# Optimization experiments

Hardware: AMD Instinct MI355X
Metric: run time of the kernel (lower is better)

Reference implementation:

```python
import jax, jax.numpy as jnp
import numpy as np

B, N = 16, 512            # graphs, atoms per graph
F_DIM, H, D = 128, 64, 16  # feature_dim, hidden_dim, far_source_dim
CUT, GROWTH = 5.0, 2.0
NS, NT = 3, 2
MULT = GROWTH ** NS        # default far_max_radius_multiplier = 8
EMAX = CUT * MULT          # 40.0
TOT = NS + NT              # 5 shells total
SF = D + 3                 # 19 per-shell features
SE_IN = TOT * SF           # 95
EH_IN = 4 * D + SE_IN      # 159
N_RBF = 8
BOUNDS = [(5.0, 10.0), (10.0, 20.0), (20.0, 40.0), (40.0, 80.0), (80.0, float('inf'))]


def ln(x, g, b):
    m = x.mean(-1, keepdims=True)
    v = x.var(-1, keepdims=True)
    return (x - m) / jnp.sqrt(v + 1e-5) * g + b


def setup_inputs() -> dict:
    key = jax.random.key(0)
    ks = jax.random.split(key, 16)
    W = lambda k, i, o: jax.random.normal(k, (i, o), jnp.float32) / np.sqrt(i)
    inp = {}
    inp['x'] = jax.random.normal(ks[0], (B * N, F_DIM), jnp.float32)
    inp['pos'] = jax.random.uniform(ks[1], (B * N, 3), jnp.float32) * 80.0
    inp['batch'] = jnp.repeat(jnp.arange(B, dtype=jnp.int32), N)
    inp['num_graphs'] = B
    inp['in_ln_g'] = jnp.ones(F_DIM); inp['in_ln_b'] = jnp.zeros(F_DIM)
    inp['src_w1'] = W(ks[2], F_DIM, H); inp['src_b1'] = jnp.zeros(H)
    inp['src_w2'] = W(ks[3], H, D);     inp['src_b2'] = jnp.zeros(D)
    inp['src_ln_g'] = jnp.ones(D); inp['src_ln_b'] = jnp.zeros(D)
    inp['se_ln_g'] = jnp.ones(SE_IN); inp['se_ln_b'] = jnp.zeros(SE_IN)
    inp['se_w1'] = W(ks[4], SE_IN, H); inp['se_b1'] = jnp.zeros(H)
    inp['se_w2'] = W(ks[5], H, D);     inp['se_b2'] = jnp.zeros(D)
    inp['eh_ln_g'] = jnp.ones(EH_IN); inp['eh_ln_b'] = jnp.zeros(EH_IN)
    inp['eh_w1'] = W(ks[6], EH_IN, H); inp['eh_b1'] = jnp.zeros(H)
    inp['eh_w2'] = W(ks[7], H, 1);     inp['eh_b2'] = jnp.zeros(1)
    inp['k_screen'] = jnp.float32(-8.0)
    inp['kg_w1'] = W(ks[8], N_RBF + 2, 32); inp['kg_b1'] = jnp.zeros(32)
    inp['kg_w2'] = jnp.zeros((32, 1)); inp['kg_b2'] = jnp.zeros(1)  # zero-init per source
    inp['far_gate'] = jnp.float32(0.2)
    inp['energy_scale'] = jnp.float32(0.0)
    return inp


def reference(x, pos, batch, num_graphs, in_ln_g, in_ln_b, src_w1, src_b1, src_w2, src_b2,
              src_ln_g, src_ln_b, se_ln_g, se_ln_b, se_w1, se_b1, se_w2, se_b2,
              eh_ln_g, eh_ln_b, eh_w1, eh_b1, eh_w2, eh_b2,
              k_screen, kg_w1, kg_b1, kg_w2, kg_b2, far_gate, energy_scale):
    M = x.shape[0]
    n = M // num_graphs
    # per-atom source features
    h = ln(x, in_ln_g, in_ln_b)
    src = jax.nn.silu(h @ src_w1 + src_b1) @ src_w2 + src_b2
    src = ln(src, src_ln_g, src_ln_b)
    # graph-wise neutralization (subtract per-graph mean)
    gsum = jax.ops.segment_sum(src, batch, num_segments=num_graphs)
    cnt = jax.ops.segment_sum(jnp.ones((M, 1), x.dtype), batch, num_segments=num_graphs)
    src = src - (gsum / jnp.maximum(cnt, 1.0))[batch]
    # pairwise distances per graph
    p = pos.reshape(num_graphs, n, 3)
    s = src.reshape(num_graphs, n, D)
    diff = p[:, :, None, :] - p[:, None, :, :]
    d = jnp.sqrt((diff * diff).sum(-1) + 1e-12)  # [B,n,n]
    not_self = ~jnp.eye(n, dtype=bool)[None]
    # physical kernel with learned RBF gate
    screening = jax.nn.softplus(k_screen)
    base = jnp.exp(-screening * d) / jnp.maximum(d, 1e-6)
    centers = jnp.linspace(CUT, EMAX, N_RBF)
    spacing = (EMAX - CUT) / (N_RBF - 1)
    gamma = 1.0 / (spacing * spacing)
    dc = d[..., None]
    rbf = jnp.exp(-gamma * (dc - centers) ** 2)
    gin = jnp.concatenate([dc / CUT, dc / EMAX, rbf], -1)
    gate = 1.0 + jnp.tanh(jax.nn.silu(gin @ kg_w1 + kg_b1) @ kg_w2 + kg_b2)[..., 0]
    ker = base * gate
    # shell statistics: kernel-weighted mean source, count, mean_r, rms_r per shell
    feats = []
    for lo, up in BOUNDS:
        m = (d >= lo) & not_self
        if np.isfinite(up):
            m = m & (d < up)
        mf = m.astype(x.dtype)
        c = mf.sum(-1)
        denom = jnp.maximum(c, 1.0)
        mean = jnp.einsum('bij,bjc->bic', ker * mf, s) / denom[..., None]
        mr = (mf * d).sum(-1) / denom
        rr = jnp.sqrt((mf * d * d).sum(-1) / denom + 1e-12)
        feats.append(jnp.concatenate([mean, c[..., None], mr[..., None], rr[..., None]], -1))
    shell = jnp.concatenate(feats, -1).reshape(M, SE_IN)  # [M, 95]
    emb = jax.nn.silu(ln(shell, se_ln_g, se_ln_b) @ se_w1 + se_b1) @ se_w2 + se_b2
    ein = jnp.concatenate([src, emb, src * emb, src - emb, shell], -1)  # [M, 159]
    pa = (jax.nn.silu(ln(ein, eh_ln_g, eh_ln_b) @ eh_w1 + eh_b1) @ eh_w2 + eh_b2)[..., 0]
    pa = pa * jnp.tanh(far_gate) * jnp.exp(energy_scale)
    return jax.ops.segment_sum(pa, batch, num_segments=num_graphs)  # per-graph energies [B]
```

## Files before the change

kernel.cpp:

```cpp
#include <hip/hip_runtime.h>
#include <math.h>

#define B_G   16
#define N_A   512
#define M_AT  8192
#define FD    128
#define HD    64
#define DD    16
#define SEIN  95
#define EHIN  159
#define NLUT  512
#define DMAXF 140.0f
#define NFB   512

__device__ __forceinline__ float silu_f(float z) { return z / (1.f + __expf(-z)); }

__global__ __launch_bounds__(256) void k_front(
    const float* __restrict__ x,
    const float* __restrict__ g, const float* __restrict__ bb,
    const float* __restrict__ w1, const float* __restrict__ b1,
    const float* __restrict__ w2, const float* __restrict__ b2,
    const float* __restrict__ lng, const float* __restrict__ lnb,
    const float* __restrict__ k_screen,
    const float* __restrict__ kg_w1, const float* __restrict__ kg_b1,
    const float* __restrict__ kg_w2, const float* __restrict__ kg_b2,
    float* __restrict__ srcout, float* __restrict__ partials,
    float2* __restrict__ lut, float* __restrict__ out) {
  int t = threadIdx.x;

  if (blockIdx.x >= NFB) {
    int lb = blockIdx.x - NFB;
    __shared__ float w1l[320], b1l[32], w2l[32];
    if (lb == 0 && t < B_G) out[t] = 0.f;
    for (int idx = t; idx < 320; idx += 256) w1l[idx] = kg_w1[idx];
    if (t < 32) { b1l[t] = kg_b1[t]; w2l[t] = kg_w2[t]; }
    __syncthreads();
    int i = lb * 256 + t;
    float step = DMAXF / (float)(NLUT - 1);
    float ksv = k_screen[0];
    float screening = fmaxf(ksv, 0.f) + log1pf(expf(-fabsf(ksv)));
    float b2v = kg_b2[0];
    float vals[2];
#pragma unroll
    for (int e = 0; e < 2; ++e) {
      int ii = min(i + e, NLUT - 1);
      float d = (float)ii * step;
      float base = expf(-screening * d) / fmaxf(d, 1e-6f);
      float gin[10];
      gin[0] = d * (1.f / 5.0f);
      gin[1] = d * (1.f / 40.0f);
#pragma unroll
      for (int kk = 0; kk < 8; ++kk) {
        float u = d - (5.0f + 5.0f * (float)kk);
        gin[2 + kk] = expf(-(1.f / 25.f) * u * u);
      }
      float accv = 0.f;
      for (int h = 0; h < 32; ++h) {
        float z = b1l[h];
#pragma unroll
        for (int kk = 0; kk < 10; ++kk) z += gin[kk] * w1l[kk * 32 + h];
        accv += silu_f(z) * w2l[h];
      }
      vals[e] = base * (1.f + tanhf(accv + b2v));
    }
    lut[i] = make_float2(vals[0], vals[1] - vals[0]);
    return;
  }

  int wave = t >> 6, lane = t & 63;
  int ag = lane >> 4, l16 = lane & 15;
  int a = wave * 4 + ag;
  int atom = blockIdx.x * 16 + a;

  __shared__ __align__(16) float xn[16 * 132];
  __shared__ __align__(16) float hb[16 * 68];
  __shared__ float psum[4][16];

  float xr[8];
  {
    const float4* xp = (const float4*)(x + (size_t)atom * FD + l16 * 8);
    float4 v0 = xp[0], v1 = xp[1];
    xr[0] = v0.x; xr[1] = v0.y; xr[2] = v0.z; xr[3] = v0.w;
    xr[4] = v1.x; xr[5] = v1.y; xr[6] = v1.z; xr[7] = v1.w;
  }
  float s = 0.f;
#pragma unroll
  for (int i = 0; i < 8; ++i) s += xr[i];
  s += __shfl_xor(s, 1); s += __shfl_xor(s, 2); s += __shfl_xor(s, 4); s += __shfl_xor(s, 8);
  float m = s * (1.f / 128.f);
  float v2 = 0.f;
#pragma unroll
  for (int i = 0; i < 8; ++i) { float d = xr[i] - m; v2 += d * d; }
  v2 += __shfl_xor(v2, 1); v2 += __shfl_xor(v2, 2); v2 += __shfl_xor(v2, 4); v2 += __shfl_xor(v2, 8);
  float inv = rsqrtf(v2 * (1.f / 128.f) + 1e-5f);
  {
    int kb = l16 * 8;
    float4 gv0 = ((const float4*)g)[l16 * 2], gv1 = ((const float4*)g)[l16 * 2 + 1];
    float4 bv0 = ((const float4*)bb)[l16 * 2], bv1 = ((const float4*)bb)[l16 * 2 + 1];
    float4 o0, o1;
    o0.x = (xr[0] - m) * inv * gv0.x + bv0.x;
    o0.y = (xr[1] - m) * inv * gv0.y + bv0.y;
    o0.z = (xr[2] - m) * inv * gv0.z + bv0.z;
    o0.w = (xr[3] - m) * inv * gv0.w + bv0.w;
    o1.x = (xr[4] - m) * inv * gv1.x + bv1.x;
    o1.y = (xr[5] - m) * inv * gv1.y + bv1.y;
    o1.z = (xr[6] - m) * inv * gv1.z + bv1.z;
    o1.w = (xr[7] - m) * inv * gv1.w + bv1.w;
    *(float4*)&xn[a * 132 + kb] = o0;
    *(float4*)&xn[a * 132 + kb + 4] = o1;
  }
  __syncthreads();

  float acc[4] = {0.f, 0.f, 0.f, 0.f};
  {
    const float* xnb = &xn[a * 132];
#pragma unroll 4
    for (int k = 0; k < FD; k += 4) {
      float4 xa = *(const float4*)(xnb + k);
      float4 wa = ((const float4*)(w1 + (size_t)(k + 0) * HD))[l16];
      float4 wbv = ((const float4*)(w1 + (size_t)(k + 1) * HD))[l16];
      float4 wc = ((const float4*)(w1 + (size_t)(k + 2) * HD))[l16];
      float4 wd = ((const float4*)(w1 + (size_t)(k + 3) * HD))[l16];
      acc[0] += wa.x * xa.x; acc[0] += wbv.x * xa.y; acc[0] += wc.x * xa.z; acc[0] += wd.x * xa.w;
      acc[1] += wa.y * xa.x; acc[1] += wbv.y * xa.y; acc[1] += wc.y * xa.z; acc[1] += wd.y * xa.w;
      acc[2] += wa.z * xa.x; acc[2] += wbv.z * xa.y; acc[2] += wc.z * xa.z; acc[2] += wd.z * xa.w;
      acc[3] += wa.w * xa.x; acc[3] += wbv.w * xa.y; acc[3] += wc.w * xa.z; acc[3] += wd.w * xa.w;
    }
    float4 bv = ((const float4*)b1)[l16];
    float4 ho;
    ho.x = silu_f(acc[0] + bv.x); ho.y = silu_f(acc[1] + bv.y);
    ho.z = silu_f(acc[2] + bv.z); ho.w = silu_f(acc[3] + bv.w);
    *(float4*)&hb[a * 68 + l16 * 4] = ho;
  }
  __syncthreads();

  {
    float acc2 = 0.f;
    const float* hbb = &hb[a * 68];
#pragma unroll
    for (int h = 0; h < HD; h += 4) {
      float4 hv = *(const float4*)(hbb + h);
      acc2 += w2[(h + 0) * DD + l16] * hv.x;
      acc2 += w2[(h + 1) * DD + l16] * hv.y;
      acc2 += w2[(h + 2) * DD + l16] * hv.z;
      acc2 += w2[(h + 3) * DD + l16] * hv.w;
    }
    float val = acc2 + b2[l16];
    float sm = val;
    sm += __shfl_xor(sm, 1); sm += __shfl_xor(sm, 2); sm += __shfl_xor(sm, 4); sm += __shfl_xor(sm, 8);
    float mm = sm * (1.f / 16.f);
    float dv = val - mm;
    float vv = dv * dv;
    vv += __shfl_xor(vv, 1); vv += __shfl_xor(vv, 2); vv += __shfl_xor(vv, 4); vv += __shfl_xor(vv, 8);
    float iv = rsqrtf(vv * (1.f / 16.f) + 1e-5f);
    float ov = dv * iv * lng[l16] + lnb[l16];
    srcout[(size_t)atom * DD + l16] = ov;
    float lsum = ov;
    lsum += __shfl_xor(lsum, 16); lsum += __shfl_xor(lsum, 32);
    if (lane < 16) psum[wave][l16] = lsum;
  }
  __syncthreads();
  if (t < 16)
    partials[(size_t)blockIdx.x * 16 + t] =
        psum[0][t] + psum[1][t] + psum[2][t] + psum[3][t];
}

__global__ __launch_bounds__(256) void k_pairs(
    const float* __restrict__ pos, const float* __restrict__ src,
    const float2* __restrict__ lut, const float* __restrict__ partials,
    float* __restrict__ shell) {
  int gph = blockIdx.x >> 7;
  int blk = blockIdx.x & 127;
  int t = threadIdx.x, wave = t >> 6, lane = t & 63;
  int i_local = blk * 4 + wave;

  __shared__ __align__(16) float ss[N_A * DD];
  __shared__ __align__(16) float2 luts[NLUT];
  __shared__ __align__(16) unsigned wb[4][N_A];
  __shared__ float smean[16];

  const float* posg = pos + (size_t)gph * N_A * 3;

  for (int idx = t; idx < N_A * DD / 4; idx += 256)
    ((float4*)ss)[idx] = ((const float4*)(src + (size_t)gph * N_A * DD))[idx];
  if (t < NLUT / 2) ((float4*)luts)[t] = ((const float4*)lut)[t];
  if (t < 64) {
    int c = t & 15, grp = t >> 4;
    float sm = 0.f;
#pragma unroll
    for (int k = 0; k < 8; ++k)
      sm += partials[(size_t)(gph * 32 + grp * 8 + k) * 16 + c];
    sm += __shfl_xor(sm, 16); sm += __shfl_xor(sm, 32);
    if (t < 16) smean[c] = sm * (1.f / 512.f);
  }

  float px = posg[i_local * 3], py = posg[i_local * 3 + 1], pz = posg[i_local * 3 + 2];
  __syncthreads();

  float cnt[5] = {0,0,0,0,0}, sd[5] = {0,0,0,0,0}, sdd[5] = {0,0,0,0,0}, sw[5] = {0,0,0,0,0};
  const float lscale = (float)(NLUT - 1) / DMAXF;

#pragma unroll
  for (int it = 0; it < 8; ++it) {
    int jv = lane + it * 64;
    float qx = posg[jv * 3], qy = posg[jv * 3 + 1], qz = posg[jv * 3 + 2];
    float dx = px - qx, dy = py - qy, dz = pz - qz;
    float d2 = dx * dx + dy * dy + dz * dz + 1e-12f;
    float d = sqrtf(d2);
    bool valid = (jv != i_local) && (d >= 5.0f);
    int tq = (d >= 10.f) + (d >= 20.f) + (d >= 40.f) + (d >= 80.f);
    float xq = d * lscale;
    int i0 = min((int)xq, NLUT - 2);
    float f = xq - (float)i0;
    float2 L = luts[i0];
    float w = valid ? (L.x + L.y * f) : 0.f;
    wb[wave][jv] = (__float_as_uint(w) & ~7u) | (unsigned)tq;
    float dm = valid ? d : 0.f;
    float ddm = valid ? d * d : 0.f;
    float cm = valid ? 1.f : 0.f;
#pragma unroll
    for (int q = 0; q < 5; ++q) {
      bool mq = (tq == q);
      cnt[q] += mq ? cm : 0.f;
      sd[q]  += mq ? dm : 0.f;
      sdd[q] += mq ? ddm : 0.f;
      sw[q]  += mq ? w : 0.f;
    }
  }
#pragma unroll
  for (int q = 0; q < 5; ++q) {
#pragma unroll
    for (int o = 32; o > 0; o >>= 1) {
      cnt[q] += __shfl_xor(cnt[q], o);
      sd[q]  += __shfl_xor(sd[q], o);
      sdd[q] += __shfl_xor(sdd[q], o);
      sw[q]  += __shfl_xor(sw[q], o);
    }
  }
  __syncthreads();

  int cq = lane & 3, jlow = lane >> 2;
  float accq[5][4] = {};
  const float* ssb = &ss[jlow * DD + cq * 4];
  const unsigned* wbb = &wb[wave][jlow];
#pragma unroll
  for (int jj = 0; jj < 32; ++jj) {
    float4 sv = *(const float4*)(ssb + jj * 256);
    unsigned u = wbb[jj * 16];
    int tq = (int)(u & 7u);
    float w = __uint_as_float(u & ~7u);
    float w0 = (tq == 0) ? w : 0.f;
    float w1_ = (tq == 1) ? w : 0.f;
    float w2_ = (tq == 2) ? w : 0.f;
    float w3_ = (tq == 3) ? w : 0.f;
    float w4_ = (tq == 4) ? w : 0.f;
    accq[0][0] += w0 * sv.x; accq[0][1] += w0 * sv.y; accq[0][2] += w0 * sv.z; accq[0][3] += w0 * sv.w;
    accq[1][0] += w1_ * sv.x; accq[1][1] += w1_ * sv.y; accq[1][2] += w1_ * sv.z; accq[1][3] += w1_ * sv.w;
    accq[2][0] += w2_ * sv.x; accq[2][1] += w2_ * sv.y; accq[2][2] += w2_ * sv.z; accq[2][3] += w2_ * sv.w;
    accq[3][0] += w3_ * sv.x; accq[3][1] += w3_ * sv.y; accq[3][2] += w3_ * sv.z; accq[3][3] += w3_ * sv.w;
    accq[4][0] += w4_ * sv.x; accq[4][1] += w4_ * sv.y; accq[4][2] += w4_ * sv.z; accq[4][3] += w4_ * sv.w;
  }
#pragma unroll
  for (int q = 0; q < 5; ++q)
#pragma unroll
    for (int i = 0; i < 4; ++i) {
      float v = accq[q][i];
      v += __shfl_xor(v, 4); v += __shfl_xor(v, 8); v += __shfl_xor(v, 16); v += __shfl_xor(v, 32);
      accq[q][i] = v;
    }

  float* shp = shell + (size_t)(gph * N_A + i_local) * SEIN;
  if (jlow == 0) {
#pragma unroll
    for (int q = 0; q < 5; ++q) {
      float denom = fmaxf(cnt[q], 1.f);
#pragma unroll
      for (int i = 0; i < 4; ++i) {
        int c = cq * 4 + i;
        shp[q * 19 + c] = (accq[q][i] - smean[c] * sw[q]) / denom;
      }
    }
  }
  if (lane < 5) {
    int q = lane;
    float denom = fmaxf(cnt[q], 1.f);
    shp[q * 19 + 16] = cnt[q];
    shp[q * 19 + 17] = sd[q] / denom;
    shp[q * 19 + 18] = sqrtf(sdd[q] / denom + 1e-12f);
  }
}

__global__ __launch_bounds__(256) void k_tail(
    const float* __restrict__ src, const float* __restrict__ shell,
    const float* __restrict__ partials,
    const float* __restrict__ se_ln_g, const float* __restrict__ se_ln_b,
    const float* __restrict__ se_w1, const float* __restrict__ se_b1,
    const float* __restrict__ se_w2, const float* __restrict__ se_b2,
    const float* __restrict__ eh_ln_g, const float* __restrict__ eh_ln_b,
    const float* __restrict__ eh_w1, const float* __restrict__ eh_b1,
    const float* __restrict__ eh_w2, const float* __restrict__ eh_b2,
    const float* __restrict__ far_gate, const float* __restrict__ energy_scale,
    float* __restrict__ out) {
  int t = threadIdx.x, wave = t >> 6, lane = t & 63;
  int ag = lane >> 4, l16 = lane & 15;
  int a = wave * 4 + ag;
  int aB = blockIdx.x * 16;
  int gph = aB >> 9;

  __shared__ __align__(16) float ein[16 * 160];
  __shared__ __align__(16) float shn[16 * 96];
  __shared__ __align__(16) float hb[16 * 68];
  __shared__ float smean[16];
  __shared__ float redv[4];

  if (t < 64) {
    int c = t & 15, grp = t >> 4;
    float sm = 0.f;
#pragma unroll
    for (int k = 0; k < 8; ++k)
      sm += partials[(size_t)(gph * 32 + grp * 8 + k) * 16 + c];
    sm += __shfl_xor(sm, 16); sm += __shfl_xor(sm, 32);
    if (t < 16) smean[c] = sm * (1.f / 512.f);
  }

  const float* shg = shell + (size_t)aB * SEIN;
  for (int idx = t; idx < 16 * SEIN; idx += 256) {
    unsigned a_loc = ((unsigned)idx * 690u) >> 16;
    int kk = idx - (int)a_loc * SEIN;
    ein[a_loc * 160 + 64 + kk] = shg[idx];
  }
  __syncthreads();

  {
    float s1 = 0.f, sq = 0.f;
    const float* eb = &ein[a * 160 + 64];
#pragma unroll
    for (int i = 0; i < 6; ++i) {
      int k = l16 * 6 + i;
      if (k < SEIN) { float v = eb[k]; s1 += v; sq += v * v; }
    }
    s1 += __shfl_xor(s1, 1); s1 += __shfl_xor(s1, 2); s1 += __shfl_xor(s1, 4); s1 += __shfl_xor(s1, 8);
    sq += __shfl_xor(sq, 1); sq += __shfl_xor(sq, 2); sq += __shfl_xor(sq, 4); sq += __shfl_xor(sq, 8);
    float m = s1 * (1.f / (float)SEIN);
    float var = sq * (1.f / (float)SEIN) - m * m;
    float inv = rsqrtf(var + 1e-5f);
#pragma unroll
    for (int i = 0; i < 6; ++i) {
      int k = l16 * 6 + i;
      if (k < SEIN)
        shn[a * 96 + k] = (eb[k] - m) * inv * se_ln_g[k] + se_ln_b[k];
    }
  }
  __syncthreads();

  int h0 = l16 * 4;
  {
    float acc[4] = {0.f, 0.f, 0.f, 0.f};
    const float* sb = &shn[a * 96];
#pragma unroll 4
    for (int k = 0; k < 92; k += 4) {
      float4 xa = *(const float4*)(sb + k);
      float4 wa = ((const float4*)(se_w1 + (size_t)(k + 0) * HD))[l16];
      float4 wbv = ((const float4*)(se_w1 + (size_t)(k + 1) * HD))[l16];
      float4 wc = ((const float4*)(se_w1 + (size_t)(k + 2) * HD))[l16];
      float4 wd = ((const float4*)(se_w1 + (size_t)(k + 3) * HD))[l16];
      acc[0] += wa.x * xa.x; acc[0] += wbv.x * xa.y; acc[0] += wc.x * xa.z; acc[0] += wd.x * xa.w;
      acc[1] += wa.y * xa.x; acc[1] += wbv.y * xa.y; acc[1] += wc.y * xa.z; acc[1] += wd.y * xa.w;
      acc[2] += wa.z * xa.x; acc[2] += wbv.z * xa.y; acc[2] += wc.z * xa.z; acc[2] += wd.z * xa.w;
      acc[3] += wa.w * xa.x; acc[3] += wbv.w * xa.y; acc[3] += wc.w * xa.z; acc[3] += wd.w * xa.w;
    }
#pragma unroll
    for (int k = 92; k < SEIN; ++k) {
      float xa = sb[k];
      float4 wa = ((const float4*)(se_w1 + (size_t)k * HD))[l16];
      acc[0] += wa.x * xa; acc[1] += wa.y * xa; acc[2] += wa.z * xa; acc[3] += wa.w * xa;
    }
    float4 bv = ((const float4*)se_b1)[l16];
    float4 ho;
    ho.x = silu_f(acc[0] + bv.x); ho.y = silu_f(acc[1] + bv.y);
    ho.z = silu_f(acc[2] + bv.z); ho.w = silu_f(acc[3] + bv.w);
    *(float4*)&hb[a * 68 + h0] = ho;
  }
  __syncthreads();

  {
    float acc2 = 0.f;
    const float* hbb = &hb[a * 68];
#pragma unroll
    for (int h = 0; h < HD; h += 4) {
      float4 hv = *(const float4*)(hbb + h);
      acc2 += se_w2[(h + 0) * DD + l16] * hv.x;
      acc2 += se_w2[(h + 1) * DD + l16] * hv.y;
      acc2 += se_w2[(h + 2) * DD + l16] * hv.z;
      acc2 += se_w2[(h + 3) * DD + l16] * hv.w;
    }
    float ev = acc2 + se_b2[l16];
    float sv = src[(size_t)(aB + a) * DD + l16] - smean[l16];
    ein[a * 160 + l16] = sv;
    ein[a * 160 + 16 + l16] = ev;
    ein[a * 160 + 32 + l16] = sv * ev;
    ein[a * 160 + 48 + l16] = sv - ev;
  }
  __syncthreads();

  {
    float s1 = 0.f, sq = 0.f;
    float* eb = &ein[a * 160];
#pragma unroll
    for (int i = 0; i < 10; ++i) {
      int k = l16 * 10 + i;
      if (k < EHIN) { float v = eb[k]; s1 += v; sq += v * v; }
    }
    s1 += __shfl_xor(s1, 1); s1 += __shfl_xor(s1, 2); s1 += __shfl_xor(s1, 4); s1 += __shfl_xor(s1, 8);
    sq += __shfl_xor(sq, 1); sq += __shfl_xor(sq, 2); sq += __shfl_xor(sq, 4); sq += __shfl_xor(sq, 8);
    float m = s1 * (1.f / (float)EHIN);
    float var = sq * (1.f / (float)EHIN) - m * m;
    float inv = rsqrtf(var + 1e-5f);
#pragma unroll
    for (int i = 0; i < 10; ++i) {
      int k = l16 * 10 + i;
      if (k < EHIN)
        eb[k] = (eb[k] - m) * inv * eh_ln_g[k] + eh_ln_b[k];
    }
  }
  __syncthreads();

  {
    float acc[4] = {0.f, 0.f, 0.f, 0.f};
    const float* eb = &ein[a * 160];
#pragma unroll 4
    for (int k = 0; k < 156; k += 4) {
      float4 xa = *(const float4*)(eb + k);
      float4 wa = ((const float4*)(eh_w1 + (size_t)(k + 0) * HD))[l16];
      float4 wbv = ((const float4*)(eh_w1 + (size_t)(k + 1) * HD))[l16];
      float4 wc = ((const float4*)(eh_w1 + (size_t)(k + 2) * HD))[l16];
      float4 wd = ((const float4*)(eh_w1 + (size_t)(k + 3) * HD))[l16];
      acc[0] += wa.x * xa.x; acc[0] += wbv.x * xa.y; acc[0] += wc.x * xa.z; acc[0] += wd.x * xa.w;
      acc[1] += wa.y * xa.x; acc[1] += wbv.y * xa.y; acc[1] += wc.y * xa.z; acc[1] += wd.y * xa.w;
      acc[2] += wa.z * xa.x; acc[2] += wbv.z * xa.y; acc[2] += wc.z * xa.z; acc[2] += wd.z * xa.w;
      acc[3] += wa.w * xa.x; acc[3] += wbv.w * xa.y; acc[3] += wc.w * xa.z; acc[3] += wd.w * xa.w;
    }
#pragma unroll
    for (int k = 156; k < EHIN; ++k) {
      float xa = eb[k];
      float4 wa = ((const float4*)(eh_w1 + (size_t)k * HD))[l16];
      acc[0] += wa.x * xa; acc[1] += wa.y * xa; acc[2] += wa.z * xa; acc[3] += wa.w * xa;
    }
    float4 b1v = ((const float4*)eh_b1)[l16];
    float4 w2v = ((const float4*)eh_w2)[l16];
    float pa = silu_f(acc[0] + b1v.x) * w2v.x + silu_f(acc[1] + b1v.y) * w2v.y
             + silu_f(acc[2] + b1v.z) * w2v.z + silu_f(acc[3] + b1v.w) * w2v.w;
    pa += __shfl_xor(pa, 1); pa += __shfl_xor(pa, 2); pa += __shfl_xor(pa, 4); pa += __shfl_xor(pa, 8);
    pa += __shfl_xor(pa, 16); pa += __shfl_xor(pa, 32);
    if (lane == 0) redv[wave] = pa + 4.f * eh_b2[0];
  }
  __syncthreads();
  if (t == 0) {
    float tot = redv[0] + redv[1] + redv[2] + redv[3];
    atomicAdd(&out[gph], tot * tanhf(far_gate[0]) * expf(energy_scale[0]));
  }
}

extern "C" void kernel_launch(void* const* d_in, const int* in_sizes, int n_in,
                              void* d_out, int out_size, void* d_ws, size_t ws_size,
                              hipStream_t stream) {
  const float* x         = (const float*)d_in[0];
  const float* pos       = (const float*)d_in[1];
  const float* in_ln_g   = (const float*)d_in[4];
  const float* in_ln_b   = (const float*)d_in[5];
  const float* src_w1    = (const float*)d_in[6];
  const float* src_b1    = (const float*)d_in[7];
  const float* src_w2    = (const float*)d_in[8];
  const float* src_b2    = (const float*)d_in[9];
  const float* src_ln_g  = (const float*)d_in[10];
  const float* src_ln_b  = (const float*)d_in[11];
  const float* se_ln_g   = (const float*)d_in[12];
  const float* se_ln_b   = (const float*)d_in[13];
  const float* se_w1     = (const float*)d_in[14];
  const float* se_b1     = (const float*)d_in[15];
  const float* se_w2     = (const float*)d_in[16];
  const float* se_b2     = (const float*)d_in[17];
  const float* eh_ln_g   = (const float*)d_in[18];
  const float* eh_ln_b   = (const float*)d_in[19];
  const float* eh_w1     = (const float*)d_in[20];
  const float* eh_b1     = (const float*)d_in[21];
  const float* eh_w2     = (const float*)d_in[22];
  const float* eh_b2     = (const float*)d_in[23];
  const float* k_screen  = (const float*)d_in[24];
  const float* kg_w1     = (const float*)d_in[25];
  const float* kg_b1     = (const float*)d_in[26];
  const float* kg_w2     = (const float*)d_in[27];
  const float* kg_b2     = (const float*)d_in[28];
  const float* far_gate  = (const float*)d_in[29];
  const float* en_scale  = (const float*)d_in[30];
  float* out = (float*)d_out;

  float* ws_src   = (float*)d_ws;
  float* ws_shell = ws_src + (size_t)M_AT * DD;
  float* ws_part  = ws_shell + (size_t)M_AT * SEIN;
  float2* ws_lut  = (float2*)(ws_part + NFB * 16);

  k_front<<<NFB + 2, 256, 0, stream>>>(x, in_ln_g, in_ln_b, src_w1, src_b1,
                                       src_w2, src_b2, src_ln_g, src_ln_b,
                                       k_screen, kg_w1, kg_b1, kg_w2, kg_b2,
                                       ws_src, ws_part, ws_lut, out);
  k_pairs<<<B_G * (N_A / 4), 256, 0, stream>>>(pos, ws_src, ws_lut, ws_part, ws_shell);
  k_tail<<<M_AT / 16, 256, 0, stream>>>(ws_src, ws_shell, ws_part,
                                        se_ln_g, se_ln_b, se_w1, se_b1, se_w2, se_b2,
                                        eh_ln_g, eh_ln_b, eh_w1, eh_b1, eh_w2, eh_b2,
                                        far_gate, en_scale, out);
}
```

Measured before the change: 189.5 us.

## Compact per-shell neighbor indices with ballots and sparse-gather shell means

The old version computed the kernel-weighted shell means by looping over all 512 neighbors, doing masked multiply-adds into five shell accumulators for every neighbor. The new version first uses wave ballots and popcounts to compact the neighbor indices of each shell into a shared-memory list. It then gathers only the members of each shell, doing four FMAs per neighbor instead of twenty. The price is extra ballot passes and dependent indirect LDS loads, and the block-wide __syncthreads before this stage is dropped. The list layout assumes the number of nonzero-weight entries in each shell equals the float shell count.

```diff
diff --git a/kernel.cpp b/kernel.cpp
--- a/kernel.cpp
+++ b/kernel.cpp
@@ -177,6 +177,7 @@
   __shared__ __align__(16) float ss[N_A * DD];
   __shared__ __align__(16) float2 luts[NLUT];
   __shared__ __align__(16) unsigned wb[4][N_A];
+  __shared__ __align__(16) unsigned short jl[4][N_A];
   __shared__ float smean[16];
 
   const float* posg = pos + (size_t)gph * N_A * 3;
@@ -237,48 +238,66 @@
       sw[q]  += __shfl_xor(sw[q], o);
     }
   }
-  __syncthreads();
-
-  int cq = lane & 3, jlow = lane >> 2;
-  float accq[5][4] = {};
-  const float* ssb = &ss[jlow * DD + cq * 4];
-  const unsigned* wbb = &wb[wave][jlow];
-#pragma unroll
-  for (int jj = 0; jj < 32; ++jj) {
-    float4 sv = *(const float4*)(ssb + jj * 256);
-    unsigned u = wbb[jj * 16];
-    int tq = (int)(u & 7u);
-    float w = __uint_as_float(u & ~7u);
-    float w0 = (tq == 0) ? w : 0.f;
-    float w1_ = (tq == 1) ? w : 0.f;
-    float w2_ = (tq == 2) ? w : 0.f;
-    float w3_ = (tq == 3) ? w : 0.f;
-    float w4_ = (tq == 4) ? w : 0.f;
-    accq[0][0] += w0 * sv.x; accq[0][1] += w0 * sv.y; accq[0][2] += w0 * sv.z; accq[0][3] += w0 * sv.w;
-    accq[1][0] += w1_ * sv.x; accq[1][1] += w1_ * sv.y; accq[1][2] += w1_ * sv.z; accq[1][3] += w1_ * sv.w;
-    accq[2][0] += w2_ * sv.x; accq[2][1] += w2_ * sv.y; accq[2][2] += w2_ * sv.z; accq[2][3] += w2_ * sv.w;
-    accq[3][0] += w3_ * sv.x; accq[3][1] += w3_ * sv.y; accq[3][2] += w3_ * sv.z; accq[3][3] += w3_ * sv.w;
-    accq[4][0] += w4_ * sv.x; accq[4][1] += w4_ * sv.y; accq[4][2] += w4_ * sv.z; accq[4][3] += w4_ * sv.w;
-  }
-#pragma unroll
-  for (int q = 0; q < 5; ++q)
-#pragma unroll
-    for (int i = 0; i < 4; ++i) {
-      float v = accq[q][i];
-      v += __shfl_xor(v, 4); v += __shfl_xor(v, 8); v += __shfl_xor(v, 16); v += __shfl_xor(v, 32);
-      accq[q][i] = v;
-    }
-
+
+  int nI[5], stq[5];
+#pragma unroll
+  for (int q = 0; q < 5; ++q) nI[q] = (int)cnt[q];
+  stq[0] = 0;
+  stq[1] = nI[0];
+  stq[2] = stq[1] + nI[1];
+  stq[3] = stq[2] + nI[2];
+  stq[4] = stq[3] + nI[3];
+  {
+    int b0 = stq[0], b1 = stq[1], b2 = stq[2], b3 = stq[3], b4 = stq[4];
+    unsigned long long lt = (lane == 63) ? 0x7fffffffffffffffull
+                                         : ((1ull << lane) - 1ull);
+#pragma unroll
+    for (int it = 0; it < 8; ++it) {
+      int jv = lane + it * 64;
+      unsigned u = wb[wave][jv];
+      int tq = (int)(u & 7u);
+      bool val = (u >> 3) != 0u;
+      unsigned long long m0 = __ballot(val && tq == 0);
+      unsigned long long m1 = __ballot(val && tq == 1);
+      unsigned long long m2 = __ballot(val && tq == 2);
+      unsigned long long m3 = __ballot(val && tq == 3);
+      unsigned long long m4 = __ballot(val && tq == 4);
+      if (val) {
+        if (tq == 0)      jl[wave][b0 + __popcll(m0 & lt)] = (unsigned short)jv;
+        else if (tq == 1) jl[wave][b1 + __popcll(m1 & lt)] = (unsigned short)jv;
+        else if (tq == 2) jl[wave][b2 + __popcll(m2 & lt)] = (unsigned short)jv;
+        else if (tq == 3) jl[wave][b3 + __popcll(m3 & lt)] = (unsigned short)jv;
+        else              jl[wave][b4 + __popcll(m4 & lt)] = (unsigned short)jv;
+      }
+      b0 += __popcll(m0); b1 += __popcll(m1); b2 += __popcll(m2);
+      b3 += __popcll(m3); b4 += __popcll(m4);
+    }
+  }
+
+  int cq = lane & 3, jl16 = lane >> 2;
   float* shp = shell + (size_t)(gph * N_A + i_local) * SEIN;
-  if (jlow == 0) {
-#pragma unroll
-    for (int q = 0; q < 5; ++q) {
+#pragma unroll
+  for (int q = 0; q < 5; ++q) {
+    float a0 = 0.f, a1 = 0.f, a2 = 0.f, a3 = 0.f;
+    int n = nI[q], s0 = stq[q];
+    for (int idx = jl16; idx < n; idx += 16) {
+      int j = jl[wave][s0 + idx];
+      unsigned u = wb[wave][j];
+      float w = __uint_as_float(u & ~7u);
+      float4 sv = *(const float4*)&ss[j * DD + cq * 4];
+      a0 += w * sv.x; a1 += w * sv.y; a2 += w * sv.z; a3 += w * sv.w;
+    }
+    a0 += __shfl_xor(a0, 4); a0 += __shfl_xor(a0, 8); a0 += __shfl_xor(a0, 16); a0 += __shfl_xor(a0, 32);
+    a1 += __shfl_xor(a1, 4); a1 += __shfl_xor(a1, 8); a1 += __shfl_xor(a1, 16); a1 += __shfl_xor(a1, 32);
+    a2 += __shfl_xor(a2, 4); a2 += __shfl_xor(a2, 8); a2 += __shfl_xor(a2, 16); a2 += __shfl_xor(a2, 32);
+    a3 += __shfl_xor(a3, 4); a3 += __shfl_xor(a3, 8); a3 += __shfl_xor(a3, 16); a3 += __shfl_xor(a3, 32);
+    if (jl16 == 0) {
       float denom = fmaxf(cnt[q], 1.f);
-#pragma unroll
-      for (int i = 0; i < 4; ++i) {
-        int c = cq * 4 + i;
-        shp[q * 19 + c] = (accq[q][i] - smean[c] * sw[q]) / denom;
-      }
+      int c = cq * 4;
+      shp[q * 19 + c + 0] = (a0 - smean[c + 0] * sw[q]) / denom;
+      shp[q * 19 + c + 1] = (a1 - smean[c + 1] * sw[q]) / denom;
+      shp[q * 19 + c + 2] = (a2 - smean[c + 2] * sw[q]) / denom;
+      shp[q * 19 + c + 3] = (a3 - smean[c + 3] * sw[q]) / denom;
     }
   }
   if (lane < 5) {
```

Result: slower. 196.5 us (+3.7%).

## Fuse tail MLP heads into pair kernel, drop shell workspace round-trip

Applied to the files above, without the earlier changes.

The per-atom shell-embedding MLP and energy head now run inside k_pairs, one wave per atom, using shared-memory staging instead of writing the 95-float shell vector to global memory and launching k_tail. This removes one kernel launch and the global write and read of the shell buffer. Each wave now does both MLPs with one hidden unit per lane and scalar weight loads, which may use the lanes less efficiently than the previous 16-atom tiled tail. It also adds shared memory to k_pairs, which may lower occupancy.

```diff
diff --git a/kernel.cpp b/kernel.cpp
--- a/kernel.cpp
+++ b/kernel.cpp
@@ -168,7 +168,14 @@
 __global__ __launch_bounds__(256) void k_pairs(
     const float* __restrict__ pos, const float* __restrict__ src,
     const float2* __restrict__ lut, const float* __restrict__ partials,
-    float* __restrict__ shell) {
+    const float* __restrict__ se_ln_g, const float* __restrict__ se_ln_b,
+    const float* __restrict__ se_w1, const float* __restrict__ se_b1,
+    const float* __restrict__ se_w2, const float* __restrict__ se_b2,
+    const float* __restrict__ eh_ln_g, const float* __restrict__ eh_ln_b,
+    const float* __restrict__ eh_w1, const float* __restrict__ eh_b1,
+    const float* __restrict__ eh_w2, const float* __restrict__ eh_b2,
+    const float* __restrict__ far_gate, const float* __restrict__ energy_scale,
+    float* __restrict__ out) {
   int gph = blockIdx.x >> 7;
   int blk = blockIdx.x & 127;
   int t = threadIdx.x, wave = t >> 6, lane = t & 63;
@@ -177,7 +184,12 @@
   __shared__ __align__(16) float ss[N_A * DD];
   __shared__ __align__(16) float2 luts[NLUT];
   __shared__ __align__(16) unsigned wb[4][N_A];
+  __shared__ __align__(16) float shl[4][100];
+  __shared__ __align__(16) float shnf[4][100];
+  __shared__ __align__(16) float einf[4][164];
+  __shared__ __align__(16) float hbf[4][64];
   __shared__ float smean[16];
+  __shared__ float redv[4];
 
   const float* posg = pos + (size_t)gph * N_A * 3;
 
@@ -239,220 +251,125 @@
   }
   __syncthreads();
 
-  int cq = lane & 3, jlow = lane >> 2;
-  float accq[5][4] = {};
-  const float* ssb = &ss[jlow * DD + cq * 4];
-  const unsigned* wbb = &wb[wave][jlow];
-#pragma unroll
-  for (int jj = 0; jj < 32; ++jj) {
-    float4 sv = *(const float4*)(ssb + jj * 256);
-    unsigned u = wbb[jj * 16];
-    int tq = (int)(u & 7u);
-    float w = __uint_as_float(u & ~7u);
-    float w0 = (tq == 0) ? w : 0.f;
-    float w1_ = (tq == 1) ? w : 0.f;
-    float w2_ = (tq == 2) ? w : 0.f;
-    float w3_ = (tq == 3) ? w : 0.f;
-    float w4_ = (tq == 4) ? w : 0.f;
-    accq[0][0] += w0 * sv.x; accq[0][1] += w0 * sv.y; accq[0][2] += w0 * sv.z; accq[0][3] += w0 * sv.w;
-    accq[1][0] += w1_ * sv.x; accq[1][1] += w1_ * sv.y; accq[1][2] += w1_ * sv.z; accq[1][3] += w1_ * sv.w;
-    accq[2][0] += w2_ * sv.x; accq[2][1] += w2_ * sv.y; accq[2][2] += w2_ * sv.z; accq[2][3] += w2_ * sv.w;
-    accq[3][0] += w3_ * sv.x; accq[3][1] += w3_ * sv.y; accq[3][2] += w3_ * sv.z; accq[3][3] += w3_ * sv.w;
-    accq[4][0] += w4_ * sv.x; accq[4][1] += w4_ * sv.y; accq[4][2] += w4_ * sv.z; accq[4][3] += w4_ * sv.w;
-  }
-#pragma unroll
-  for (int q = 0; q < 5; ++q)
-#pragma unroll
-    for (int i = 0; i < 4; ++i) {
-      float v = accq[q][i];
-      v += __shfl_xor(v, 4); v += __shfl_xor(v, 8); v += __shfl_xor(v, 16); v += __shfl_xor(v, 32);
-      accq[q][i] = v;
-    }
-
-  float* shp = shell + (size_t)(gph * N_A + i_local) * SEIN;
-  if (jlow == 0) {
-#pragma unroll
-    for (int q = 0; q < 5; ++q) {
+  {
+    int cq = lane & 3, jlow = lane >> 2;
+    float accq[5][4] = {};
+    const float* ssb = &ss[jlow * DD + cq * 4];
+    const unsigned* wbb = &wb[wave][jlow];
+#pragma unroll
+    for (int jj = 0; jj < 32; ++jj) {
+      float4 sv = *(const float4*)(ssb + jj * 256);
+      unsigned u = wbb[jj * 16];
+      int tq = (int)(u & 7u);
+      float w = __uint_as_float(u & ~7u);
+      float w0 = (tq == 0) ? w : 0.f;
+      float w1_ = (tq == 1) ? w : 0.f;
+      float w2_ = (tq == 2) ? w : 0.f;
+      float w3_ = (tq == 3) ? w : 0.f;
+      float w4_ = (tq == 4) ? w : 0.f;
+      accq[0][0] += w0 * sv.x; accq[0][1] += w0 * sv.y; accq[0][2] += w0 * sv.z; accq[0][3] += w0 * sv.w;
+      accq[1][0] += w1_ * sv.x; accq[1][1] += w1_ * sv.y; accq[1][2] += w1_ * sv.z; accq[1][3] += w1_ * sv.w;
+      accq[2][0] += w2_ * sv.x; accq[2][1] += w2_ * sv.y; accq[2][2] += w2_ * sv.z; accq[2][3] += w2_ * sv.w;
+      accq[3][0] += w3_ * sv.x; accq[3][1] += w3_ * sv.y; accq[3][2] += w3_ * sv.z; accq[3][3] += w3_ * sv.w;
+      accq[4][0] += w4_ * sv.x; accq[4][1] += w4_ * sv.y; accq[4][2] += w4_ * sv.z; accq[4][3] += w4_ * sv.w;
+    }
+#pragma unroll
+    for (int q = 0; q < 5; ++q)
+#pragma unroll
+      for (int i = 0; i < 4; ++i) {
+        float v = accq[q][i];
+        v += __shfl_xor(v, 4); v += __shfl_xor(v, 8); v += __shfl_xor(v, 16); v += __shfl_xor(v, 32);
+        accq[q][i] = v;
+      }
+
+    if (jlow == 0) {
+#pragma unroll
+      for (int q = 0; q < 5; ++q) {
+        float denom = fmaxf(cnt[q], 1.f);
+#pragma unroll
+        for (int i = 0; i < 4; ++i) {
+          int c = cq * 4 + i;
+          shl[wave][q * 19 + c] = (accq[q][i] - smean[c] * sw[q]) / denom;
+        }
+      }
+    }
+    if (lane < 5) {
+      int q = lane;
       float denom = fmaxf(cnt[q], 1.f);
-#pragma unroll
-      for (int i = 0; i < 4; ++i) {
-        int c = cq * 4 + i;
-        shp[q * 19 + c] = (accq[q][i] - smean[c] * sw[q]) / denom;
-      }
-    }
-  }
-  if (lane < 5) {
-    int q = lane;
-    float denom = fmaxf(cnt[q], 1.f);
-    shp[q * 19 + 16] = cnt[q];
-    shp[q * 19 + 17] = sd[q] / denom;
-    shp[q * 19 + 18] = sqrtf(sdd[q] / denom + 1e-12f);
-  }
-}
-
-__global__ __launch_bounds__(256) void k_tail(
-    const float* __restrict__ src, const float* __restrict__ shell,
-    const float* __restrict__ partials,
-    const float* __restrict__ se_ln_g, const float* __restrict__ se_ln_b,
-    const float* __restrict__ se_w1, const float* __restrict__ se_b1,
-    const float* __restrict__ se_w2, const float* __restrict__ se_b2,
-    const float* __restrict__ eh_ln_g, const float* __restrict__ eh_ln_b,
-    const float* __restrict__ eh_w1, const float* __restrict__ eh_b1,
-    const float* __restrict__ eh_w2, const float* __restrict__ eh_b2,
-    const float* __restrict__ far_gate, const float* __restrict__ energy_scale,
-    float* __restrict__ out) {
-  int t = threadIdx.x, wave = t >> 6, lane = t & 63;
-  int ag = lane >> 4, l16 = lane & 15;
-  int a = wave * 4 + ag;
-  int aB = blockIdx.x * 16;
-  int gph = aB >> 9;
-
-  __shared__ __align__(16) float ein[16 * 160];
-  __shared__ __align__(16) float shn[16 * 96];
-  __shared__ __align__(16) float hb[16 * 68];
-  __shared__ float smean[16];
-  __shared__ float redv[4];
-
-  if (t < 64) {
-    int c = t & 15, grp = t >> 4;
-    float sm = 0.f;
-#pragma unroll
-    for (int k = 0; k < 8; ++k)
-      sm += partials[(size_t)(gph * 32 + grp * 8 + k) * 16 + c];
-    sm += __shfl_xor(sm, 16); sm += __shfl_xor(sm, 32);
-    if (t < 16) smean[c] = sm * (1.f / 512.f);
-  }
-
-  const float* shg = shell + (size_t)aB * SEIN;
-  for (int idx = t; idx < 16 * SEIN; idx += 256) {
-    unsigned a_loc = ((unsigned)idx * 690u) >> 16;
-    int kk = idx - (int)a_loc * SEIN;
-    ein[a_loc * 160 + 64 + kk] = shg[idx];
-  }
-  __syncthreads();
-
-  {
-    float s1 = 0.f, sq = 0.f;
-    const float* eb = &ein[a * 160 + 64];
-#pragma unroll
-    for (int i = 0; i < 6; ++i) {
-      int k = l16 * 6 + i;
-      if (k < SEIN) { float v = eb[k]; s1 += v; sq += v * v; }
-    }
-    s1 += __shfl_xor(s1, 1); s1 += __shfl_xor(s1, 2); s1 += __shfl_xor(s1, 4); s1 += __shfl_xor(s1, 8);
-    sq += __shfl_xor(sq, 1); sq += __shfl_xor(sq, 2); sq += __shfl_xor(sq, 4); sq += __shfl_xor(sq, 8);
+      shl[wave][q * 19 + 16] = cnt[q];
+      shl[wave][q * 19 + 17] = sd[q] / denom;
+      shl[wave][q * 19 + 18] = sqrtf(sdd[q] / denom + 1e-12f);
+    }
+  }
+  __syncthreads();
+
+  {
+    float v1 = shl[wave][lane];
+    float v2 = (lane < 31) ? shl[wave][lane + 64] : 0.f;
+    float s1 = v1 + v2, sq = v1 * v1 + v2 * v2;
+    s1 += __shfl_xor(s1, 1); s1 += __shfl_xor(s1, 2); s1 += __shfl_xor(s1, 4);
+    s1 += __shfl_xor(s1, 8); s1 += __shfl_xor(s1, 16); s1 += __shfl_xor(s1, 32);
+    sq += __shfl_xor(sq, 1); sq += __shfl_xor(sq, 2); sq += __shfl_xor(sq, 4);
+    sq += __shfl_xor(sq, 8); sq += __shfl_xor(sq, 16); sq += __shfl_xor(sq, 32);
     float m = s1 * (1.f / (float)SEIN);
     float var = sq * (1.f / (float)SEIN) - m * m;
     float inv = rsqrtf(var + 1e-5f);
-#pragma unroll
-    for (int i = 0; i < 6; ++i) {
-      int k = l16 * 6 + i;
-      if (k < SEIN)
-        shn[a * 96 + k] = (eb[k] - m) * inv * se_ln_g[k] + se_ln_b[k];
-    }
-  }
-  __syncthreads();
-
-  int h0 = l16 * 4;
-  {
-    float acc[4] = {0.f, 0.f, 0.f, 0.f};
-    const float* sb = &shn[a * 96];
-#pragma unroll 4
-    for (int k = 0; k < 92; k += 4) {
-      float4 xa = *(const float4*)(sb + k);
-      float4 wa = ((const float4*)(se_w1 + (size_t)(k + 0) * HD))[l16];
-      float4 wbv = ((const float4*)(se_w1 + (size_t)(k + 1) * HD))[l16];
-      float4 wc = ((const float4*)(se_w1 + (size_t)(k + 2) * HD))[l16];
-      float4 wd = ((const float4*)(se_w1 + (size_t)(k + 3) * HD))[l16];
-      acc[0] += wa.x * xa.x; acc[0] += wbv.x * xa.y; acc[0] += wc.x * xa.z; acc[0] += wd.x * xa.w;
-      acc[1] += wa.y * xa.x; acc[1] += wbv.y * xa.y; acc[1] += wc.y * xa.z; acc[1] += wd.y * xa.w;
-      acc[2] += wa.z * xa.x; acc[2] += wbv.z * xa.y; acc[2] += wc.z * xa.z; acc[2] += wd.z * xa.w;
-      acc[3] += wa.w * xa.x; acc[3] += wbv.w * xa.y; acc[3] += wc.w * xa.z; acc[3] += wd.w * xa.w;
-    }
-#pragma unroll
-    for (int k = 92; k < SEIN; ++k) {
-      float xa = sb[k];
-      float4 wa = ((const float4*)(se_w1 + (size_t)k * HD))[l16];
-      acc[0] += wa.x * xa; acc[1] += wa.y * xa; acc[2] += wa.z * xa; acc[3] += wa.w * xa;
-    }
-    float4 bv = ((const float4*)se_b1)[l16];
-    float4 ho;
-    ho.x = silu_f(acc[0] + bv.x); ho.y = silu_f(acc[1] + bv.y);
-    ho.z = silu_f(acc[2] + bv.z); ho.w = silu_f(acc[3] + bv.w);
-    *(float4*)&hb[a * 68 + h0] = ho;
-  }
-  __syncthreads();
-
-  {
+    shnf[wave][lane] = (v1 - m) * inv * se_ln_g[lane] + se_ln_b[lane];
+    einf[wave][64 + lane] = v1;
+    if (lane < 31) {
+      shnf[wave][lane + 64] = (v2 - m) * inv * se_ln_g[lane + 64] + se_ln_b[lane + 64];
+      einf[wave][128 + lane] = v2;
+    }
+  }
+
+  {
+    float acc = 0.f;
+#pragma unroll 5
+    for (int k = 0; k < SEIN; ++k)
+      acc += shnf[wave][k] * se_w1[(size_t)k * HD + lane];
+    hbf[wave][lane] = silu_f(acc + se_b1[lane]);
+  }
+
+  if (lane < 16) {
     float acc2 = 0.f;
-    const float* hbb = &hb[a * 68];
-#pragma unroll
-    for (int h = 0; h < HD; h += 4) {
-      float4 hv = *(const float4*)(hbb + h);
-      acc2 += se_w2[(h + 0) * DD + l16] * hv.x;
-      acc2 += se_w2[(h + 1) * DD + l16] * hv.y;
-      acc2 += se_w2[(h + 2) * DD + l16] * hv.z;
-      acc2 += se_w2[(h + 3) * DD + l16] * hv.w;
-    }
-    float ev = acc2 + se_b2[l16];
-    float sv = src[(size_t)(aB + a) * DD + l16] - smean[l16];
-    ein[a * 160 + l16] = sv;
-    ein[a * 160 + 16 + l16] = ev;
-    ein[a * 160 + 32 + l16] = sv * ev;
-    ein[a * 160 + 48 + l16] = sv - ev;
-  }
-  __syncthreads();
-
-  {
-    float s1 = 0.f, sq = 0.f;
-    float* eb = &ein[a * 160];
-#pragma unroll
-    for (int i = 0; i < 10; ++i) {
-      int k = l16 * 10 + i;
-      if (k < EHIN) { float v = eb[k]; s1 += v; sq += v * v; }
-    }
-    s1 += __shfl_xor(s1, 1); s1 += __shfl_xor(s1, 2); s1 += __shfl_xor(s1, 4); s1 += __shfl_xor(s1, 8);
-    sq += __shfl_xor(sq, 1); sq += __shfl_xor(sq, 2); sq += __shfl_xor(sq, 4); sq += __shfl_xor(sq, 8);
+#pragma unroll 8
+    for (int h = 0; h < HD; ++h)
+      acc2 += hbf[wave][h] * se_w2[h * DD + lane];
+    float ev = acc2 + se_b2[lane];
+    float sv = ss[i_local * DD + lane] - smean[lane];
+    einf[wave][lane] = sv;
+    einf[wave][16 + lane] = ev;
+    einf[wave][32 + lane] = sv * ev;
+    einf[wave][48 + lane] = sv - ev;
+  }
+
+  {
+    float v1 = einf[wave][lane];
+    float v2 = einf[wave][64 + lane];
+    float v3 = (lane < 31) ? einf[wave][128 + lane] : 0.f;
+    float s1 = v1 + v2 + v3, sq = v1 * v1 + v2 * v2 + v3 * v3;
+    s1 += __shfl_xor(s1, 1); s1 += __shfl_xor(s1, 2); s1 += __shfl_xor(s1, 4);
+    s1 += __shfl_xor(s1, 8); s1 += __shfl_xor(s1, 16); s1 += __shfl_xor(s1, 32);
+    sq += __shfl_xor(sq, 1); sq += __shfl_xor(sq, 2); sq += __shfl_xor(sq, 4);
+    sq += __shfl_xor(sq, 8); sq += __shfl_xor(sq, 16); sq += __shfl_xor(sq, 32);
     float m = s1 * (1.f / (float)EHIN);
     float var = sq * (1.f / (float)EHIN) - m * m;
     float inv = rsqrtf(var + 1e-5f);
-#pragma unroll
-    for (int i = 0; i < 10; ++i) {
-      int k = l16 * 10 + i;
-      if (k < EHIN)
-        eb[k] = (eb[k] - m) * inv * eh_ln_g[k] + eh_ln_b[k];
-    }
-  }
-  __syncthreads();
-
-  {
-    float acc[4] = {0.f, 0.f, 0.f, 0.f};
-    const float* eb = &ein[a * 160];
-#pragma unroll 4
-    for (int k = 0; k < 156; k += 4) {
-      float4 xa = *(const float4*)(eb + k);
-      float4 wa = ((const float4*)(eh_w1 + (size_t)(k + 0) * HD))[l16];
-      float4 wbv = ((const float4*)(eh_w1 + (size_t)(k + 1) * HD))[l16];
-      float4 wc = ((const float4*)(eh_w1 + (size_t)(k + 2) * HD))[l16];
-      float4 wd = ((const float4*)(eh_w1 + (size_t)(k + 3) * HD))[l16];
-      acc[0] += wa.x * xa.x; acc[0] += wbv.x * xa.y; acc[0] += wc.x * xa.z; acc[0] += wd.x * xa.w;
-      acc[1] += wa.y * xa.x; acc[1] += wbv.y * xa.y; acc[1] += wc.y * xa.z; acc[1] += wd.y * xa.w;
-      acc[2] += wa.z * xa.x; acc[2] += wbv.z * xa.y; acc[2] += wc.z * xa.z; acc[2] += wd.z * xa.w;
-      acc[3] += wa.w * xa.x; acc[3] += wbv.w * xa.y; acc[3] += wc.w * xa.z; acc[3] += wd.w * xa.w;
-    }
-#pragma unroll
-    for (int k = 156; k < EHIN; ++k) {
-      float xa = eb[k];
-      float4 wa = ((const float4*)(eh_w1 + (size_t)k * HD))[l16];
-      acc[0] += wa.x * xa; acc[1] += wa.y * xa; acc[2] += wa.z * xa; acc[3] += wa.w * xa;
-    }
-    float4 b1v = ((const float4*)eh_b1)[l16];
-    float4 w2v = ((const float4*)eh_w2)[l16];
-    float pa = silu_f(acc[0] + b1v.x) * w2v.x + silu_f(acc[1] + b1v.y) * w2v.y
-             + silu_f(acc[2] + b1v.z) * w2v.z + silu_f(acc[3] + b1v.w) * w2v.w;
-    pa += __shfl_xor(pa, 1); pa += __shfl_xor(pa, 2); pa += __shfl_xor(pa, 4); pa += __shfl_xor(pa, 8);
-    pa += __shfl_xor(pa, 16); pa += __shfl_xor(pa, 32);
-    if (lane == 0) redv[wave] = pa + 4.f * eh_b2[0];
+    einf[wave][lane] = (v1 - m) * inv * eh_ln_g[lane] + eh_ln_b[lane];
+    einf[wave][64 + lane] = (v2 - m) * inv * eh_ln_g[64 + lane] + eh_ln_b[64 + lane];
+    if (lane < 31)
+      einf[wave][128 + lane] = (v3 - m) * inv * eh_ln_g[128 + lane] + eh_ln_b[128 + lane];
+  }
+
+  {
+    float acc = 0.f;
+#pragma unroll 3
+    for (int k = 0; k < EHIN; ++k)
+      acc += einf[wave][k] * eh_w1[(size_t)k * HD + lane];
+    float pa = silu_f(acc + eh_b1[lane]) * eh_w2[lane];
+    pa += __shfl_xor(pa, 1); pa += __shfl_xor(pa, 2); pa += __shfl_xor(pa, 4);
+    pa += __shfl_xor(pa, 8); pa += __shfl_xor(pa, 16); pa += __shfl_xor(pa, 32);
+    if (lane == 0) redv[wave] = pa + eh_b2[0];
   }
   __syncthreads();
   if (t == 0) {
@@ -496,17 +413,16 @@
   float* out = (float*)d_out;
 
   float* ws_src   = (float*)d_ws;
-  float* ws_shell = ws_src + (size_t)M_AT * DD;
-  float* ws_part  = ws_shell + (size_t)M_AT * SEIN;
+  float* ws_part  = ws_src + (size_t)M_AT * DD;
   float2* ws_lut  = (float2*)(ws_part + NFB * 16);
 
   k_front<<<NFB + 2, 256, 0, stream>>>(x, in_ln_g, in_ln_b, src_w1, src_b1,
                                        src_w2, src_b2, src_ln_g, src_ln_b,
                                        k_screen, kg_w1, kg_b1, kg_w2, kg_b2,
                                        ws_src, ws_part, ws_lut, out);
-  k_pairs<<<B_G * (N_A / 4), 256, 0, stream>>>(pos, ws_src, ws_lut, ws_part, ws_shell);
-  k_tail<<<M_AT / 16, 256, 0, stream>>>(ws_src, ws_shell, ws_part,
-                                        se_ln_g, se_ln_b, se_w1, se_b1, se_w2, se_b2,
-                                        eh_ln_g, eh_ln_b, eh_w1, eh_b1, eh_w2, eh_b2,
-                                        far_gate, en_scale, out);
+  k_pairs<<<B_G * (N_A / 4), 256, 0, stream>>>(
+      pos, ws_src, ws_lut, ws_part,
+      se_ln_g, se_ln_b, se_w1, se_b1, se_w2, se_b2,
+      eh_ln_g, eh_ln_b, eh_w1, eh_b1, eh_w2, eh_b2,
+      far_gate, en_scale, out);
 }
```

Result: slower. 216.6 us (+14.3%).
